# Kernel tuning notes

Hardware: AMD Instinct MI355X
Metric: run time of the kernel (lower is better)

The kernel has to match this reference:

```python
import jax, jax.numpy as jnp
import numpy as np

B, T, C = 2, 2048, 2048
NH = 16            # query heads
NKV = NH // 2      # kv heads (GQA)
HD = C // NH       # head dim = 128
N_REP = NH // NKV  # 2


def setup_inputs() -> dict:
    key = jax.random.key(0)
    k1, k2, k3 = jax.random.split(key, 3)
    x = jax.random.normal(k1, (B, T, C), jnp.float32)
    w_attn = jax.random.normal(k2, (C, (NH + 2 * NKV) * HD), jnp.float32) * 0.02
    w_proj = jax.random.normal(k3, (C, C), jnp.float32) * 0.02
    t = jnp.arange(T, dtype=jnp.float32)
    inv_freq = 1.0 / (10000.0 ** (jnp.arange(0, HD, 2, dtype=jnp.float32) / HD))
    freqs = t[:, None] * inv_freq[None, :]  # [T, HD//2]
    return {"x": x, "w_attn": w_attn, "w_proj": w_proj,
            "freqs_cos": jnp.cos(freqs), "freqs_sin": jnp.sin(freqs)}


def _rope(v, cos, sin):
    # v: [B, T, H, HD]; complex multiply on (even, odd) pairs
    vr = v.reshape(*v.shape[:-1], HD // 2, 2)
    x0, x1 = vr[..., 0], vr[..., 1]
    c = cos[None, :, None, :]
    s = sin[None, :, None, :]
    o0 = x0 * c - x1 * s
    o1 = x0 * s + x1 * c
    return jnp.stack([o0, o1], axis=-1).reshape(v.shape)


def reference(x, w_attn, w_proj, freqs_cos, freqs_sin):
    qkv = x @ w_attn  # [B, T, (NH+2*NKV)*HD]
    q, k, v = jnp.split(qkv, [NH * HD, (NH + NKV) * HD], axis=-1)
    q = q.reshape(B, T, NH, HD)
    k = k.reshape(B, T, NKV, HD)
    v = v.reshape(B, T, NKV, HD)
    q = _rope(q, freqs_cos, freqs_sin)
    k = _rope(k, freqs_cos, freqs_sin)
    # GQA: group query heads over kv heads instead of repeating k/v
    q = q.transpose(0, 2, 1, 3).reshape(B, NKV, N_REP, T, HD)  # [B, G, R, T, HD]
    k = k.transpose(0, 2, 1, 3)  # [B, G, T, HD]
    v = v.transpose(0, 2, 1, 3)  # [B, G, T, HD]
    scale = jnp.float32(1.0 / np.sqrt(HD))
    scores = jnp.einsum('bgrqd,bgkd->bgrqk', q, k) * scale
    causal = jnp.tril(jnp.ones((T, T), dtype=bool))
    scores = jnp.where(causal, scores, jnp.float32(-1e30))
    p = jax.nn.softmax(scores, axis=-1)
    y = jnp.einsum('bgrqk,bgkd->bgrqd', p, v)  # [B, G, R, T, HD]
    y = y.reshape(B, NH, T, HD).transpose(0, 2, 1, 3).reshape(B, T, C)
    return y @ w_proj
```

## Files before the change

### kernel.cpp

```cpp
#include <hip/hip_runtime.h>
#include <hip/hip_bf16.h>
#include <stdint.h>
#include <stddef.h>

typedef unsigned short u16;
using bf16x8 = __attribute__((ext_vector_type(8))) short;
using f32x4  = __attribute__((ext_vector_type(4))) float;
using f32x16 = __attribute__((ext_vector_type(16))) float;

#define DEVFN static __device__ __forceinline__

DEVFN u16 f2b(float f){ __hip_bfloat16 h = __float2bfloat16(f); return *reinterpret_cast<u16*>(&h); }
DEVFN float b2f(u16 u){ __hip_bfloat16 h; *reinterpret_cast<u16*>(&h) = u; return __bfloat162float(h); }
DEVFN uint32_t pk2(float a, float b){
  uint32_t r; asm("v_cvt_pk_bf16_f32 %0, %1, %2" : "=v"(r) : "v"(a), "v"(b)); return r;
}
DEVFN float ex2(float x){ float r; asm("v_exp_f32 %0, %1" : "=v"(r) : "v"(x)); return r; }

DEVFN void gload_lds16(const void* g, void* l){
  __builtin_amdgcn_global_load_lds(
      (const __attribute__((address_space(1))) void*)g,
      (__attribute__((address_space(3))) void*)l, 16, 0, 0);
}

__global__ void detect_k(const uint32_t* __restrict__ fc_raw, uint32_t* __restrict__ flag){
  if (threadIdx.x == 0 && blockIdx.x == 0)
    flag[0] = (fc_raw[0] == 0x3F800000u) ? 1u : 0u;
}

__global__ __launch_bounds__(256) void cvtf_k(const void* __restrict__ in, float* __restrict__ out,
                                              int n, const uint32_t* __restrict__ flag){
  const int i = blockIdx.x*256 + threadIdx.x;
  if (i >= n) return;
  if (flag[0]) out[i] = ((const float*)in)[i];
  else         out[i] = b2f(((const u16*)in)[i]);
}

__global__ __launch_bounds__(256) void cvtx_k(const void* __restrict__ in, u16* __restrict__ out,
                                              int n8, const uint32_t* __restrict__ flag){
  const int i = blockIdx.x*256 + threadIdx.x;
  if (i >= n8) return;
  __align__(16) u16 e[8];
  if (flag[0]){
    const float* f = (const float*)in + (size_t)i*8;
    float4 a = *(const float4*)f, b = *(const float4*)(f+4);
    e[0]=f2b(a.x); e[1]=f2b(a.y); e[2]=f2b(a.z); e[3]=f2b(a.w);
    e[4]=f2b(b.x); e[5]=f2b(b.y); e[6]=f2b(b.z); e[7]=f2b(b.w);
  } else {
    *(uint4*)e = *((const uint4*)in + i);
  }
  *(uint4*)(out + (size_t)i*8) = *(const uint4*)e;
}

__global__ __launch_bounds__(512) void wtrans_k(const void* __restrict__ in, u16* __restrict__ out,
                                                int C, int R, const uint32_t* __restrict__ flag){
  __shared__ __align__(16) u16 tile[64][72];
  const int r0 = blockIdx.y*64, c0 = blockIdx.x*64;
  const int t = threadIdx.x, r = t>>3, cs = (t&7)*8;
  __align__(16) u16 e[8];
  if (flag[0]){
    const float* f = (const float*)in + (size_t)(r0+r)*C + c0 + cs;
    float4 a = *(const float4*)f, b = *(const float4*)(f+4);
    e[0]=f2b(a.x); e[1]=f2b(a.y); e[2]=f2b(a.z); e[3]=f2b(a.w);
    e[4]=f2b(b.x); e[5]=f2b(b.y); e[6]=f2b(b.z); e[7]=f2b(b.w);
  } else {
    *(uint4*)e = *(const uint4*)((const u16*)in + (size_t)(r0+r)*C + c0 + cs);
  }
#pragma unroll
  for (int j=0;j<8;j++) tile[cs+j][r] = e[j];
  __syncthreads();
  uint4 o = *(const uint4*)&tile[r][cs];
  *(uint4*)(out + (size_t)(c0+r)*R + r0 + cs) = o;
}

__global__ __launch_bounds__(512) void vtrans_k(const u16* __restrict__ qkv, u16* __restrict__ vT){
  __shared__ __align__(16) u16 tile[64][72];
  const int z = blockIdx.z, b = z>>3, g = z&7;
  const u16* in = qkv + (size_t)(b*2048)*4096 + 3072 + g*128;
  u16* out = vT + (size_t)z*128*2048;
  const int r0 = blockIdx.y*64, c0 = blockIdx.x*64;
  const int t = threadIdx.x, r = t>>3, cs = (t&7)*8;
  uint4 v = *(const uint4*)(in + (size_t)(r0+r)*4096 + c0 + cs);
  const u16* e = (const u16*)&v;
#pragma unroll
  for (int j=0;j<8;j++) tile[cs+j][r] = e[j];
  __syncthreads();
  uint4 o = *(const uint4*)&tile[r][cs];
  *(uint4*)(out + (size_t)(c0+r)*2048 + r0 + cs) = o;
}

__global__ __launch_bounds__(256) void rope_k(u16* qkv, const float* __restrict__ fc,
                                              const float* __restrict__ fs){
  const int idx = blockIdx.x*256 + threadIdx.x;
  const int row = idx / 1536;
  const int p   = idx % 1536;
  const int col0 = p*2;
  const int t = row & 2047;
  const int i = p & 63;
  uint32_t* ptr = (uint32_t*)(qkv + (size_t)row*4096 + col0);
  uint32_t u = *ptr;
  float x0 = b2f((u16)(u & 0xffff));
  float x1 = b2f((u16)(u >> 16));
  float c = fc[t*64+i], s = fs[t*64+i];
  float o0 = x0*c - x1*s;
  float o1 = x0*s + x1*c;
  if (col0 < 2048){
    const float S2 = 0.08838834764831845f * 1.4426950408889634f;
    o0 *= S2; o1 *= S2;
  }
  *ptr = (uint32_t)f2b(o0) | ((uint32_t)f2b(o1) << 16);
}

__global__ __launch_bounds__(512) void gemm_p(const u16* __restrict__ A, const u16* __restrict__ Bt,
                                              void* __restrict__ Cv, int M, int N, int K,
                                              const uint32_t* __restrict__ flag, int fin){
  __shared__ __align__(16) u16 L[3*12288];
  const int nwg_x = N>>7;
  int wg = blockIdx.x;
  { const int cpx = (int)gridDim.x >> 3; wg = (wg&7)*cpx + (wg>>3); }
  const int tm = (wg / nwg_x)*256, tn = (wg % nwg_x)*128;
  const int tid = threadIdx.x, w = tid>>6, l = tid&63, lr = l&15, lg = l>>4;
  const int wm = w>>1, wn = w&1;

  f32x4 acc[4][4] = {};

  auto stage = [&](int kt, int buf){
    const int kk = kt*32;
    u16* Lb = &L[buf*12288];
#pragma unroll
    for (int j=0;j<2;j++){
      const int s = j*512 + tid;
      const int row = s>>2, c = s&3;
      const int gch = c ^ ((row ^ (row>>2)) & 3);
      gload_lds16(A + (size_t)(tm + row)*K + kk + gch*8, &Lb[(j*512 + w*64)*8]);
    }
    {
      const int s = tid;
      const int row = s>>2, c = s&3;
      const int gch = c ^ ((row ^ (row>>2)) & 3);
      gload_lds16(Bt + (size_t)(tn + row)*K + kk + gch*8, &Lb[8192 + (w*64)*8]);
    }
  };

  const int nk = K>>5;
  stage(0,0); stage(1,1);
  asm volatile("s_waitcnt vmcnt(3)" ::: "memory");
  __builtin_amdgcn_s_barrier();
  __builtin_amdgcn_sched_barrier(0);

  for (int kt=0; kt<nk; ++kt){
    const int buf = kt % 3;
    if (kt+2 < nk) stage(kt+2, (kt+2) % 3);
    const u16* Ab = &L[buf*12288];
    const u16* Bb = Ab + 8192;
    bf16x8 a[4], b[4];
#pragma unroll
    for (int mi=0;mi<4;mi++){
      const int row = wm*64 + mi*16 + lr;
      a[mi] = *(const bf16x8*)&Ab[row*32 + ((lg ^ ((row ^ (row>>2))&3))*8)];
    }
#pragma unroll
    for (int ni=0;ni<4;ni++){
      const int row = wn*64 + ni*16 + lr;
      b[ni] = *(const bf16x8*)&Bb[row*32 + ((lg ^ ((row ^ (row>>2))&3))*8)];
    }
#pragma unroll
    for (int mi=0;mi<4;mi++)
#pragma unroll
      for (int ni=0;ni<4;ni++)
        acc[mi][ni] = __builtin_amdgcn_mfma_f32_16x16x32_bf16(a[mi], b[ni], acc[mi][ni], 0,0,0);
    __builtin_amdgcn_sched_barrier(0);
    if (kt+2 < nk) asm volatile("s_waitcnt vmcnt(3)" ::: "memory");
    else           asm volatile("s_waitcnt vmcnt(0)" ::: "memory");
    __builtin_amdgcn_s_barrier();
    __builtin_amdgcn_sched_barrier(0);
  }

  const bool of32 = fin && (flag[0] != 0);
#pragma unroll
  for (int mi=0;mi<4;mi++)
#pragma unroll
    for (int ni=0;ni<4;ni++)
#pragma unroll
      for (int reg=0;reg<4;reg++){
        const int row = tm + wm*64 + mi*16 + lg*4 + reg;
        const int col = tn + wn*64 + ni*16 + lr;
        const size_t idx = (size_t)row*N + col;
        const float v = acc[mi][ni][reg];
        if (of32) ((float*)Cv)[idx] = v;
        else      ((u16*)Cv)[idx]   = f2b(v);
      }
}

__global__ __launch_bounds__(512, 1) void attn_k(const u16* __restrict__ qkv,
                                                 const u16* __restrict__ vT,
                                                 u16* __restrict__ y){
  __shared__ __align__(16) u16 KV[2][2][16384];
  const int i0 = blockIdx.x;
  const int g  = i0 & 7;
  const int r1 = i0 >> 3;
  const int hl = r1 & 1;
  const int vq = (r1 >> 1) & 7;
  const int b  = r1 >> 4;
  const int h  = g*2 + hl;

  const int tid = threadIdx.x;
  const int w = tid >> 6, l = tid & 63;
  const int grp = w >> 2, wq = w & 3;
  const int lq = l & 31;
  const int hi = l >> 5;

  const u16* kg = qkv + (size_t)(b*2048)*4096 + 2048 + g*128;
  const u16* vg = vT  + (size_t)(b*8+g)*128*2048;

  const int rk = tid >> 2, cb = tid & 3;
  uint4 kpre[4], vpre[4];
  auto loadT = [&](int kvbase){
#pragma unroll
    for (int j=0;j<4;j++){
      const int ch = cb + j*4;
      kpre[j] = *(const uint4*)(kg + (size_t)(kvbase + rk)*4096 + ch*8);
      vpre[j] = *(const uint4*)(vg + (size_t)rk*2048 + kvbase + ch*8);
    }
  };
  auto writeT = [&](int buf){
    u16* Kd = &KV[buf][rk>>6][0];
    const int rl = rk & 63;
#pragma unroll
    for (int j=0;j<4;j++){
      const int ch = cb + j*4;
      *(uint4*)&Kd[rl*128 + ((ch ^ (rl&15))*8)] = kpre[j];
    }
#pragma unroll
    for (int j=0;j<4;j++){
      const int ch = cb + j*4;
      u16* Vd = &KV[buf][ch>>3][8192];
      *(uint4*)&Vd[rk*64 + (((ch&7) ^ (rk&7))*8)] = vpre[j];
    }
  };

  int qt = vq;
  const int nA = vq + 1;
  bf16x8 qf[8];
  f32x16 yacc[4];
  float mrow, lsum;

  auto loadQ = [&]{
    const size_t qrow = (size_t)(b*2048 + qt*128 + wq*32 + lq);
    const u16* qp = qkv + qrow*4096 + h*128 + hi*8;
#pragma unroll
    for (int ds=0; ds<8; ++ds) qf[ds] = *(const bf16x8*)(qp + ds*16);
  };
  auto resetAcc = [&]{
#pragma unroll
    for (int dt=0; dt<4; ++dt)
#pragma unroll
      for (int r=0; r<16; ++r) yacc[dt][r] = 0.f;
    mrow = -1e30f; lsum = 0.f;
  };

  auto mergePhase = [&](u16* Mb){
    float* Mm = (float*)Mb; float* Ml = Mm + 128;
    u16* MOs = Mb + 512 + wq*4096;
    __syncthreads();
    if (grp == 1){
      if (l < 32){ Mm[wq*32 + l] = mrow; Ml[wq*32 + l] = lsum; }
#pragma unroll
      for (int dt=0; dt<4; ++dt)
#pragma unroll
        for (int rq=0; rq<4; ++rq){
          const int d0 = dt*32 + rq*8 + hi*4;
          uint32_t lo = pk2(yacc[dt][rq*4+0], yacc[dt][rq*4+1]);
          uint32_t hi2= pk2(yacc[dt][rq*4+2], yacc[dt][rq*4+3]);
          const int idx = (lq*128 + d0) ^ ((lq&7)<<3);
          *(uint2*)&MOs[idx] = make_uint2(lo, hi2);
        }
    }
    __syncthreads();
    if (grp == 0){
      const float mo = Mm[wq*32 + lq], lo_ = Ml[wq*32 + lq];
      const float ms = fmaxf(mrow, mo);
      const float ce = ex2(mrow - ms), co = ex2(mo - ms);
      const float inv = 1.f / (lsum*ce + lo_*co);
#pragma unroll
      for (int dt=0; dt<4; ++dt)
#pragma unroll
        for (int rq=0; rq<4; ++rq){
          const int d0 = dt*32 + rq*8 + hi*4;
          const int idx = (lq*128 + d0) ^ ((lq&7)<<3);
          uint2 pr = *(const uint2*)&MOs[idx];
          const float yo0 = b2f((u16)(pr.x & 0xffff)), yo1 = b2f((u16)(pr.x >> 16));
          const float yo2 = b2f((u16)(pr.y & 0xffff)), yo3 = b2f((u16)(pr.y >> 16));
          uint32_t lo = pk2((yacc[dt][rq*4+0]*ce + yo0*co)*inv, (yacc[dt][rq*4+1]*ce + yo1*co)*inv);
          uint32_t hi2= pk2((yacc[dt][rq*4+2]*ce + yo2*co)*inv, (yacc[dt][rq*4+3]*ce + yo3*co)*inv);
          *(uint2*)&MOs[idx] = make_uint2(lo, hi2);
        }
    }
    __syncthreads();
    const int qb2 = b*2048 + qt*128 + wq*32;
#pragma unroll
    for (int p=0; p<2; ++p){
      const int row = grp*16 + p*8 + (l>>3);
      const int gc = l & 7;
      const int idx0 = (row*128 + gc*16) ^ ((row&7)<<3);
      const int idx1 = (row*128 + gc*16 + 8) ^ ((row&7)<<3);
      uint4 v0 = *(const uint4*)&MOs[idx0];
      uint4 v1 = *(const uint4*)&MOs[idx1];
      u16* yp = y + (size_t)(qb2 + row)*2048 + h*128 + gc*16;
      *(uint4*)yp = v0;
      *(uint4*)(yp + 8) = v1;
    }
    __syncthreads();
  };

  loadT(0); writeT(0); __syncthreads();
  loadQ(); resetAcc();

  for (int s=0; s<17; ++s){
    if (s == nA){
      mergePhase(&KV[(nA&1)^1][0][0]);
      qt = 15 - vq;
      loadQ(); resetAcc();
    }
    const int sj = (s < nA) ? s : s - nA;
    const int kvbase = sj*128;
    if (s+1 < 17){
      const int s2 = s+1;
      const int sj2 = (s2 < nA) ? s2 : s2 - nA;
      loadT(sj2*128);
    }
    const u16* Kb = &KV[s&1][grp][0];
    const u16* Vb = Kb + 8192;
    const int tilebase = kvbase + grp*64;
    const int qmin = qt*128 + wq*32;
    const int qrow = qmin + lq;

    if (tilebase <= qmin + 31){
      f32x16 sc[2];
#pragma unroll
      for (int t=0;t<2;t++)
#pragma unroll
        for (int r=0;r<16;r++) sc[t][r] = 0.f;
      __builtin_amdgcn_s_setprio(1);
#pragma unroll
      for (int t=0; t<2; ++t){
        const int r = t*32 + lq;
        const int rsw = r & 15;
#pragma unroll
        for (int ds=0; ds<8; ++ds){
          const bf16x8 kf = *(const bf16x8*)&Kb[r*128 + (((2*ds+hi) ^ rsw)*8)];
          sc[t] = __builtin_amdgcn_mfma_f32_32x32x16_bf16(kf, qf[ds], sc[t], 0,0,0);
        }
      }
      __builtin_amdgcn_s_setprio(0);

      if (tilebase + 63 > qmin){
#pragma unroll
        for (int t=0;t<2;t++)
#pragma unroll
          for (int r=0;r<16;r++){
            const int kp = tilebase + t*32 + (r&3) + 8*(r>>2) + 4*hi;
            if (kp > qrow) sc[t][r] = -1e30f;
          }
      }

      float mx[16];
#pragma unroll
      for (int r=0;r<16;r++) mx[r] = fmaxf(sc[0][r], sc[1][r]);
#pragma unroll
      for (int off=8; off>0; off>>=1)
#pragma unroll
        for (int r=0;r<8;r++)
          if (r < off) mx[r] = fmaxf(mx[r], mx[r+off]);
      float pmax = fmaxf(mx[0], __shfl_xor(mx[0], 32));

      if (!__all(pmax <= mrow + 8.f)){
        const float mnew = fmaxf(mrow, pmax);
        const float corr = ex2(mrow - mnew);
        mrow = mnew; lsum *= corr;
#pragma unroll
        for (int dt=0;dt<4;dt++)
#pragma unroll
          for (int r=0;r<16;r++) yacc[dt][r] *= corr;
      }

#pragma unroll
      for (int t=0;t<2;t++)
#pragma unroll
        for (int r=0;r<16;r++) sc[t][r] = ex2(sc[t][r] - mrow);
      float sm[16];
#pragma unroll
      for (int r=0;r<16;r++) sm[r] = sc[0][r] + sc[1][r];
#pragma unroll
      for (int off=8; off>0; off>>=1)
#pragma unroll
        for (int r=0;r<8;r++)
          if (r < off) sm[r] += sm[r+off];
      lsum += sm[0] + __shfl_xor(sm[0], 32);

      __align__(16) uint32_t pw[4][4];
#pragma unroll
      for (int t=0;t<2;t++)
#pragma unroll
        for (int half=0; half<2; ++half){
          const int q8 = half*8;
          const uint32_t X0 = pk2(sc[t][q8+0], sc[t][q8+1]);
          const uint32_t X1 = pk2(sc[t][q8+2], sc[t][q8+3]);
          const uint32_t X2 = pk2(sc[t][q8+4], sc[t][q8+5]);
          const uint32_t X3 = pk2(sc[t][q8+6], sc[t][q8+7]);
          const uint32_t pX0 = (uint32_t)__shfl_xor((int)X0, 32);
          const uint32_t pX1 = (uint32_t)__shfl_xor((int)X1, 32);
          const uint32_t pX2 = (uint32_t)__shfl_xor((int)X2, 32);
          const uint32_t pX3 = (uint32_t)__shfl_xor((int)X3, 32);
          const int ks = t*2 + half;
          pw[ks][0] = hi ? pX2 : X0;
          pw[ks][1] = hi ? pX3 : X1;
          pw[ks][2] = hi ? X2 : pX0;
          pw[ks][3] = hi ? X3 : pX1;
        }

      __builtin_amdgcn_s_setprio(1);
#pragma unroll
      for (int dt=0; dt<4; ++dt){
        const int d = dt*32 + lq;
        const int dsw = d & 7;
#pragma unroll
        for (int ks=0; ks<4; ++ks){
          const bf16x8 vf = *(const bf16x8*)&Vb[d*64 + (((2*ks+hi) ^ dsw)*8)];
          yacc[dt] = __builtin_amdgcn_mfma_f32_32x32x16_bf16(vf, *(const bf16x8*)&pw[ks][0], yacc[dt], 0,0,0);
        }
      }
      __builtin_amdgcn_s_setprio(0);
    }

    if (s+1 < 17) writeT((s&1)^1);
    __syncthreads();
  }
  mergePhase(&KV[0][0][0]);
}

extern "C" void kernel_launch(void* const* d_in, const int* in_sizes, int n_in,
                              void* d_out, int out_size, void* d_ws, size_t ws_size,
                              hipStream_t stream){
  char* ws = (char*)d_ws;
  const size_t MB = 1048576;
  uint32_t* flag = (uint32_t*)(ws);
  float* fcF = (float*)(ws + 1*MB);
  float* fsF = (float*)(ws + 1*MB + 524288);
  u16* xb   = (u16*)(ws + 2*MB);
  u16* waT  = (u16*)(ws + 18*MB);
  u16* wpT  = (u16*)(ws + 34*MB);
  u16* qkvb = (u16*)(ws + 42*MB);
  u16* vTb  = (u16*)(ws + 74*MB);
  u16* yb   = xb;

  detect_k<<<1, 64, 0, stream>>>((const uint32_t*)d_in[3], flag);
  cvtf_k  <<<512, 256, 0, stream>>>(d_in[3], fcF, 131072, flag);
  cvtf_k  <<<512, 256, 0, stream>>>(d_in[4], fsF, 131072, flag);
  cvtx_k  <<<4096, 256, 0, stream>>>(d_in[0], xb, 1048576, flag);
  wtrans_k<<<dim3(64,32,1), 512, 0, stream>>>(d_in[1], waT, 4096, 2048, flag);
  wtrans_k<<<dim3(32,32,1), 512, 0, stream>>>(d_in[2], wpT, 2048, 2048, flag);
  gemm_p  <<<dim3(512,1,1), 512, 0, stream>>>(xb, waT, qkvb, 4096, 4096, 2048, flag, 0);
  rope_k  <<<dim3(24576,1,1), 256, 0, stream>>>(qkvb, fcF, fsF);
  vtrans_k<<<dim3(2,32,16), 512, 0, stream>>>(qkvb, vTb);
  attn_k  <<<dim3(256,1,1), 512, 0, stream>>>(qkvb, vTb, yb);
  gemm_p  <<<dim3(256,1,1), 512, 0, stream>>>(yb, wpT, d_out, 4096, 2048, 2048, flag, 1);
}
```

Baseline: 271.4 us.

## Use 256x256 tiled triple-buffered GEMM for QKV projection

```diff
diff --git a/kernel.cpp b/kernel.cpp
--- a/kernel.cpp
+++ b/kernel.cpp
@@ -192,6 +192,88 @@
       }
 }
 
+__global__ __launch_bounds__(512) void gemm_p2(const u16* __restrict__ A, const u16* __restrict__ Bt,
+                                               void* __restrict__ Cv, int M, int N, int K,
+                                               const uint32_t* __restrict__ flag, int fin){
+  __shared__ __align__(16) u16 L[3*16384];
+  const int nwg_x = N>>8;
+  int wg = blockIdx.x;
+  { const int cpx = (int)gridDim.x >> 3; wg = (wg&7)*cpx + (wg>>3); }
+  const int tm = (wg / nwg_x)*256, tn = (wg % nwg_x)*256;
+  const int tid = threadIdx.x, w = tid>>6, l = tid&63, lr = l&15, lg = l>>4;
+  const int wm = w>>2, wn = w&3;
+
+  f32x4 acc[8][4] = {};
+
+  auto stage = [&](int kt, int buf){
+    const int kk = kt*32;
+    u16* Lb = &L[buf*16384];
+#pragma unroll
+    for (int j=0;j<2;j++){
+      const int s = j*512 + tid;
+      const int row = s>>2, c = s&3;
+      const int gch = c ^ ((row ^ (row>>2)) & 3);
+      gload_lds16(A + (size_t)(tm + row)*K + kk + gch*8, &Lb[(j*512 + w*64)*8]);
+    }
+#pragma unroll
+    for (int j=0;j<2;j++){
+      const int s = j*512 + tid;
+      const int row = s>>2, c = s&3;
+      const int gch = c ^ ((row ^ (row>>2)) & 3);
+      gload_lds16(Bt + (size_t)(tn + row)*K + kk + gch*8, &Lb[8192 + (j*512 + w*64)*8]);
+    }
+  };
+
+  const int nk = K>>5;
+  stage(0,0); stage(1,1);
+  asm volatile("s_waitcnt vmcnt(4)" ::: "memory");
+  __builtin_amdgcn_s_barrier();
+  __builtin_amdgcn_sched_barrier(0);
+
+  for (int kt=0; kt<nk; ++kt){
+    const int buf = kt % 3;
+    if (kt+2 < nk) stage(kt+2, (kt+2) % 3);
+    const u16* Ab = &L[buf*16384];
+    const u16* Bb = Ab + 8192;
+    bf16x8 a[8], b[4];
+#pragma unroll
+    for (int mi=0;mi<8;mi++){
+      const int row = wm*128 + mi*16 + lr;
+      a[mi] = *(const bf16x8*)&Ab[row*32 + ((lg ^ ((row ^ (row>>2))&3))*8)];
+    }
+#pragma unroll
+    for (int ni=0;ni<4;ni++){
+      const int row = wn*64 + ni*16 + lr;
+      b[ni] = *(const bf16x8*)&Bb[row*32 + ((lg ^ ((row ^ (row>>2))&3))*8)];
+    }
+#pragma unroll
+    for (int mi=0;mi<8;mi++)
+#pragma unroll
+      for (int ni=0;ni<4;ni++)
+        acc[mi][ni] = __builtin_amdgcn_mfma_f32_16x16x32_bf16(a[mi], b[ni], acc[mi][ni], 0,0,0);
+    __builtin_amdgcn_sched_barrier(0);
+    if (kt+2 < nk) asm volatile("s_waitcnt vmcnt(4)" ::: "memory");
+    else           asm volatile("s_waitcnt vmcnt(0)" ::: "memory");
+    __builtin_amdgcn_s_barrier();
+    __builtin_amdgcn_sched_barrier(0);
+  }
+
+  const bool of32 = fin && (flag[0] != 0);
+#pragma unroll
+  for (int mi=0;mi<8;mi++)
+#pragma unroll
+    for (int ni=0;ni<4;ni++)
+#pragma unroll
+      for (int reg=0;reg<4;reg++){
+        const int row = tm + wm*128 + mi*16 + lg*4 + reg;
+        const int col = tn + wn*64 + ni*16 + lr;
+        const size_t idx = (size_t)row*N + col;
+        const float v = acc[mi][ni][reg];
+        if (of32) ((float*)Cv)[idx] = v;
+        else      ((u16*)Cv)[idx]   = f2b(v);
+      }
+}
+
 __global__ __launch_bounds__(512, 1) void attn_k(const u16* __restrict__ qkv,
                                                  const u16* __restrict__ vT,
                                                  u16* __restrict__ y){
@@ -460,7 +542,7 @@
   cvtx_k  <<<4096, 256, 0, stream>>>(d_in[0], xb, 1048576, flag);
   wtrans_k<<<dim3(64,32,1), 512, 0, stream>>>(d_in[1], waT, 4096, 2048, flag);
   wtrans_k<<<dim3(32,32,1), 512, 0, stream>>>(d_in[2], wpT, 2048, 2048, flag);
-  gemm_p  <<<dim3(512,1,1), 512, 0, stream>>>(xb, waT, qkvb, 4096, 4096, 2048, flag, 0);
+  gemm_p2 <<<dim3(256,1,1), 512, 0, stream>>>(xb, waT, qkvb, 4096, 4096, 2048, flag, 0);
   rope_k  <<<dim3(24576,1,1), 256, 0, stream>>>(qkvb, fcF, fsF);
   vtrans_k<<<dim3(2,32,16), 512, 0, stream>>>(qkvb, vTb);
   attn_k  <<<dim3(256,1,1), 512, 0, stream>>>(qkvb, vTb, yb);
```

New measurement: 260.1 us. 1.04x faster.
